# Performance work log

Hardware: AMD Instinct MI355X
Metric: run time of the kernel (lower is better)

The kernel has to match this reference:

```python
import jax, jax.numpy as jnp
import numpy as np

N_NODES = 50000
N_EDGES = 400000
HID = 64
NUM_REL = 230
NUM_TS = 365
SLOPE = 0.2  # LeakyReLU negative slope

def lrelu(v):
    return jnp.where(v >= 0, v, SLOPE * v)

def setup_inputs() -> dict:
    key = jax.random.key(0)
    ks = jax.random.split(key, 10)
    x = jax.random.normal(ks[0], (N_NODES, 2 * HID), dtype=jnp.float32)
    rel_table = jax.random.normal(ks[1], (NUM_REL, HID), dtype=jnp.float32) * 0.1
    time_table = jax.random.normal(ks[2], (NUM_TS, HID), dtype=jnp.float32) * 0.1
    W_rt = jax.random.normal(ks[3], (2 * HID, 2 * HID), dtype=jnp.float32) * (1.0 / np.sqrt(2 * HID))
    b_rt = jnp.zeros((2 * HID,), dtype=jnp.float32)
    W_fc = jax.random.normal(ks[4], (6 * HID, 2 * HID), dtype=jnp.float32) * (1.0 / np.sqrt(6 * HID))
    b_fc = jnp.zeros((2 * HID,), dtype=jnp.float32)
    src = jax.random.randint(ks[5], (N_EDGES,), 0, N_NODES)
    dst = jax.random.randint(ks[6], (N_EDGES,), 0, N_NODES)
    rel = jax.random.randint(ks[7], (N_EDGES,), 0, NUM_REL)
    ts = jax.random.randint(ks[8], (N_EDGES,), 0, NUM_TS)
    edges = jnp.stack([src, dst, rel, ts], axis=1).astype(jnp.int64) if jax.config.jax_enable_x64 else jnp.stack([src, dst, rel, ts], axis=1)
    return {
        "x": x, "rel_table": rel_table, "time_table": time_table,
        "W_rt": W_rt, "b_rt": b_rt, "W_fc": W_fc, "b_fc": b_fc,
        "edges": edges, "num_nodes": N_NODES,
    }

def reference(x, rel_table, time_table, W_rt, b_rt, W_fc, b_fc, edges, num_nodes):
    # MessagePassing.forward + LogicalGNN.aggregated_messages (scatter_mean)
    src, dst, rel, ts = edges[:, 0], edges[:, 1], edges[:, 2], edges[:, 3]
    rel_e = rel_table[rel]          # [E, H]
    time_e = time_table[ts]         # [E, H]
    rel_t = lrelu(jnp.concatenate([rel_e, time_e], axis=-1) @ W_rt + b_rt)  # [E, 2H]
    msg_in = jnp.concatenate([x[src], rel_t, x[dst]], axis=-1)              # [E, 6H]
    messages = lrelu(msg_in @ W_fc + b_fc)                                  # [E, 2H]
    # scatter_mean over dst
    sums = jax.ops.segment_sum(messages, dst, num_segments=num_nodes)       # [N, 2H]
    counts = jax.ops.segment_sum(jnp.ones((messages.shape[0],), messages.dtype), dst, num_segments=num_nodes)
    agg = sums / jnp.maximum(counts, 1.0)[:, None]
    return agg
```

## Files before the change

kernel.cpp:

```cpp
#include <hip/hip_runtime.h>
#include <cstdio>

#define HID 64
#define D 128
#define NUM_REL 230
#define NUM_TS 365
#define NCOMB (NUM_REL*NUM_TS)
#define SLOPE 0.2f
#define XPAD 136
#define MAXDEG 64

typedef __attribute__((ext_vector_type(8))) short short8;
typedef __attribute__((ext_vector_type(4))) float f32x4;

__device__ __forceinline__ float lrelu(float v){ return v >= 0.f ? v : SLOPE*v; }

__device__ __forceinline__ unsigned bf_rne(float f){
    unsigned u = __float_as_uint(f);
    return (u + 0x7fffu + ((u >> 16) & 1u)) >> 16;
}
__device__ __forceinline__ unsigned pk2(float a, float b){
    return bf_rne(a) | (bf_rne(b) << 16);
}
__device__ __forceinline__ float bf_lo(unsigned u){ return __uint_as_float(u << 16); }
__device__ __forceinline__ float bf_hi(unsigned u){ return __uint_as_float(u & 0xffff0000u); }

__global__ __launch_bounds__(256) void k_prep(
        const float* __restrict__ rel_table, const float* __restrict__ time_table,
        const float* __restrict__ W_rt, const float* __restrict__ W_fc,
        const int* __restrict__ edges, int n_edges,
        float* __restrict__ relP, float* __restrict__ timP,
        unsigned short* __restrict__ Wpk13, unsigned short* __restrict__ Wpk2,
        int* __restrict__ deg, int2* __restrict__ ebuf)
{
    int b = blockIdx.x;
    if (b < 298) {
        int row = b*2 + (threadIdx.x >> 7);
        int j   = threadIdx.x & 127;
        if (row >= NUM_REL + NUM_TS) return;
        const float* tbl; const float* Wb; float* out;
        if (row < NUM_REL) { tbl = rel_table + row*HID;            Wb = W_rt;          out = relP + row*D; }
        else               { tbl = time_table + (row-NUM_REL)*HID; Wb = W_rt + HID*D;  out = timP + (row-NUM_REL)*D; }
        float acc = 0.f;
        #pragma unroll
        for (int k = 0; k < HID; ++k) acc += tbl[k] * Wb[k*D + j];
        out[j] = acc;
    } else if (b < 322) {
        int id = (b - 298)*256 + threadIdx.x;
        if (id < 4096) {
            int mt = id >> 8;
            int s  = (id >> 6) & 3;
            int l  = id & 63;
            int m  = mt*16 + (l & 15);
            int kb = s*32 + (l >> 4)*8;
            unsigned short* dst = Wpk13 + ((size_t)(mt*4 + s)*64 + l)*8;
            #pragma unroll
            for (int j = 0; j < 8; ++j) {
                int k = kb + j;
                float v = (m < D) ? W_fc[(size_t)k*D + m]
                                  : W_fc[(size_t)(256 + k)*D + (m - D)];
                dst[j] = (unsigned short)bf_rne(v);
            }
        } else {
            int id2 = id - 4096;
            int mt = id2 >> 8;
            int s  = (id2 >> 6) & 3;
            int l  = id2 & 63;
            int m  = mt*16 + (l & 15);
            int kb = s*32 + (l >> 4)*8;
            unsigned short* dst = Wpk2 + ((size_t)(mt*4 + s)*64 + l)*8;
            #pragma unroll
            for (int j = 0; j < 8; ++j) {
                int k = kb + j;
                dst[j] = (unsigned short)bf_rne(W_fc[(size_t)(D + k)*D + m]);
            }
        }
    } else {
        int e = (b - 322)*256 + threadIdx.x;
        if (e < n_edges) {
            int4 ed = ((const int4*)edges)[e];
            int slot = atomicAdd(&deg[ed.y], 1);
            if (slot < MAXDEG)
                ebuf[(size_t)ed.y*MAXDEG + slot] = make_int2(ed.x, ed.z*NUM_TS + ed.w);
        }
    }
}

__device__ __forceinline__ void xw_body(
        int xb, const float* __restrict__ x,
        const unsigned short* __restrict__ Wpk13,
        unsigned short* __restrict__ xW13bf, int n_nodes,
        unsigned short* Xs )
{
    int t = threadIdx.x;
    int nodeBase = xb*64;
    {
        int row = t >> 2;
        int k0  = (t & 3)*32;
        int node = nodeBase + row;
        unsigned short* dst = Xs + row*XPAD + k0;
        if (node < n_nodes) {
            const float4* src = (const float4*)(x + (size_t)node*D + k0);
            #pragma unroll
            for (int g = 0; g < 8; ++g) {
                float4 v = src[g];
                *(uint2*)(dst + g*4) = make_uint2(pk2(v.x, v.y), pk2(v.z, v.w));
            }
        } else {
            #pragma unroll
            for (int g = 0; g < 8; ++g)
                *(uint2*)(dst + g*4) = make_uint2(0u, 0u);
        }
    }
    __syncthreads();

    int w = t >> 6, l = t & 63;
    int li = l & 15, q = l >> 4;

    f32x4 acc[4][4];
    #pragma unroll
    for (int mi = 0; mi < 4; ++mi)
        #pragma unroll
        for (int ni = 0; ni < 4; ++ni) acc[mi][ni] = (f32x4){0.f,0.f,0.f,0.f};

    #pragma unroll 1
    for (int s = 0; s < 4; ++s) {
        short8 af[4], bf[4];
        #pragma unroll
        for (int mi = 0; mi < 4; ++mi) {
            int mt = w*4 + mi;
            af[mi] = *(const short8*)(Wpk13 + ((size_t)(mt*4 + s)*64 + l)*8);
        }
        #pragma unroll
        for (int ni = 0; ni < 4; ++ni)
            bf[ni] = *(const short8*)(Xs + (ni*16 + li)*XPAD + s*32 + q*8);
        #pragma unroll
        for (int mi = 0; mi < 4; ++mi)
            #pragma unroll
            for (int ni = 0; ni < 4; ++ni)
                acc[mi][ni] = __builtin_amdgcn_mfma_f32_16x16x32_bf16(
                                  af[mi], bf[ni], acc[mi][ni], 0, 0, 0);
    }
    #pragma unroll
    for (int ni = 0; ni < 4; ++ni) {
        int node = nodeBase + ni*16 + li;
        if (node >= n_nodes) continue;
        #pragma unroll
        for (int mi = 0; mi < 4; ++mi) {
            int col = w*64 + mi*16 + q*4;
            *(uint2*)(xW13bf + (size_t)node*256 + col) =
                make_uint2(pk2(acc[mi][ni][0], acc[mi][ni][1]),
                           pk2(acc[mi][ni][2], acc[mi][ni][3]));
        }
    }
}

__device__ __forceinline__ void t2_body(
        int tb, const float* __restrict__ relP, const float* __restrict__ timP,
        const float* __restrict__ b_rt, const unsigned short* __restrict__ Wpk2,
        unsigned short* __restrict__ T2bf,
        unsigned short* Hs )
{
    int t = threadIdx.x;
    int cBase = tb*128;
    {
        int r  = t >> 1;
        int hk = (t & 1)*64;
        int combo = cBase + r;
        if (combo >= NCOMB) combo = NCOMB - 1;
        int rr = combo / NUM_TS;
        int tt = combo - rr*NUM_TS;
        const float4* rv4 = (const float4*)(relP + (size_t)rr*D + hk);
        const float4* tv4 = (const float4*)(timP + (size_t)tt*D + hk);
        const float4* bv4 = (const float4*)(b_rt + hk);
        unsigned short* dst = Hs + r*XPAD + hk;
        #pragma unroll
        for (int g = 0; g < 16; ++g) {
            float4 rv = rv4[g], tv = tv4[g], bv = bv4[g];
            float v0 = lrelu(rv.x+tv.x+bv.x), v1 = lrelu(rv.y+tv.y+bv.y);
            float v2 = lrelu(rv.z+tv.z+bv.z), v3 = lrelu(rv.w+tv.w+bv.w);
            *(uint2*)(dst + g*4) = make_uint2(pk2(v0,v1), pk2(v2,v3));
        }
    }
    __syncthreads();

    int w = t >> 6, l = t & 63;
    int li = l & 15, q = l >> 4;
    int mb = (w & 1)*4;
    int nb = (w >> 1)*64;

    f32x4 acc[4][4];
    #pragma unroll
    for (int mi = 0; mi < 4; ++mi)
        #pragma unroll
        for (int ni = 0; ni < 4; ++ni) acc[mi][ni] = (f32x4){0.f,0.f,0.f,0.f};

    #pragma unroll 1
    for (int s = 0; s < 4; ++s) {
        short8 af[4], bf[4];
        #pragma unroll
        for (int mi = 0; mi < 4; ++mi)
            af[mi] = *(const short8*)(Wpk2 + ((size_t)((mb+mi)*4 + s)*64 + l)*8);
        #pragma unroll
        for (int ni = 0; ni < 4; ++ni)
            bf[ni] = *(const short8*)(Hs + (nb + ni*16 + li)*XPAD + s*32 + q*8);
        #pragma unroll
        for (int mi = 0; mi < 4; ++mi)
            #pragma unroll
            for (int ni = 0; ni < 4; ++ni)
                acc[mi][ni] = __builtin_amdgcn_mfma_f32_16x16x32_bf16(
                                  af[mi], bf[ni], acc[mi][ni], 0, 0, 0);
    }
    #pragma unroll
    for (int ni = 0; ni < 4; ++ni) {
        int combo = cBase + nb + ni*16 + li;
        if (combo >= NCOMB) continue;
        #pragma unroll
        for (int mi = 0; mi < 4; ++mi) {
            int col = (mb + mi)*16 + q*4;
            *(uint2*)(T2bf + (size_t)combo*D + col) =
                make_uint2(pk2(acc[mi][ni][0], acc[mi][ni][1]),
                           pk2(acc[mi][ni][2], acc[mi][ni][3]));
        }
    }
}

__global__ __launch_bounds__(256, 3) void k_mm(
        const float* __restrict__ x, const unsigned short* __restrict__ Wpk13,
        unsigned short* __restrict__ xW13bf, int n_nodes,
        const float* __restrict__ relP, const float* __restrict__ timP,
        const float* __restrict__ b_rt, const unsigned short* __restrict__ Wpk2,
        unsigned short* __restrict__ T2bf, int nxw)
{
    __shared__ __align__(16) unsigned short Hs[128*XPAD];
    int b = blockIdx.x;
    if (b < nxw) {
        xw_body(b, x, Wpk13, xW13bf, n_nodes, Hs);
    } else {
        t2_body(b - nxw, relP, timP, b_rt, Wpk2, T2bf, Hs);
    }
}

__global__ __launch_bounds__(256) void k_agg(
        const int* __restrict__ deg, const int2* __restrict__ ebuf,
        const unsigned short* __restrict__ xW13bf,
        const unsigned short* __restrict__ T2bf,
        const float* __restrict__ b_fc,
        float* __restrict__ out, int n_nodes)
{
    int node = blockIdx.x*4 + (threadIdx.x >> 6);
    int lane = threadIdx.x & 63;
    if (node >= n_nodes) return;
    int dg  = deg[node];
    int cnt = dg < MAXDEG ? dg : MAXDEG;
    const int2* eb = ebuf + (size_t)node*MAXDEG;

    float2 bb = *(const float2*)&b_fc[2*lane];
    unsigned xw3 = *(const unsigned*)&xW13bf[(size_t)node*256 + 128 + 2*lane];
    float base0 = bf_lo(xw3) + bb.x;
    float base1 = bf_hi(xw3) + bb.y;

    float s0 = 0.f, s1 = 0.f;
    float r0 = 0.f, r1 = 0.f;

    for (int e = 0; e < cnt; e += 16) {
        int m = cnt - e;
        int2 ed[16]; unsigned sv[16], tv[16];
        #pragma unroll
        for (int j = 0; j < 16; ++j)
            if (j < m) ed[j] = eb[e + j];
        #pragma unroll
        for (int j = 0; j < 16; ++j)
            if (j < m) {
                sv[j] = *(const unsigned*)&xW13bf[(size_t)ed[j].x*256 + 2*lane];
                tv[j] = *(const unsigned*)&T2bf  [(size_t)ed[j].y*D   + 2*lane];
            }
        #pragma unroll
        for (int j = 0; j < 16; ++j)
            if (j < m) {
                if (j & 1) {
                    r0 += lrelu(bf_lo(sv[j]) + bf_lo(tv[j]) + base0);
                    r1 += lrelu(bf_hi(sv[j]) + bf_hi(tv[j]) + base1);
                } else {
                    s0 += lrelu(bf_lo(sv[j]) + bf_lo(tv[j]) + base0);
                    s1 += lrelu(bf_hi(sv[j]) + bf_hi(tv[j]) + base1);
                }
            }
    }
    float inv = 1.f / fmaxf((float)dg, 1.f);
    *(float2*)&out[(size_t)node*D + 2*lane] =
        make_float2((s0 + r0)*inv, (s1 + r1)*inv);
}

extern "C" void kernel_launch(void* const* d_in, const int* in_sizes, int n_in,
                              void* d_out, int out_size, void* d_ws, size_t ws_size,
                              hipStream_t stream)
{
    const float* x          = (const float*)d_in[0];
    const float* rel_table  = (const float*)d_in[1];
    const float* time_table = (const float*)d_in[2];
    const float* W_rt       = (const float*)d_in[3];
    const float* b_rt       = (const float*)d_in[4];
    const float* W_fc       = (const float*)d_in[5];
    const float* b_fc       = (const float*)d_in[6];
    const int*   edges      = (const int*)d_in[7];

    int n_nodes = in_sizes[0] / D;
    int n_edges = in_sizes[7] / 4;
    int nblkE   = (n_edges + 255) / 256;
    int nxw     = (n_nodes + 63) / 64;
    int nt2     = (NCOMB + 127) / 128;

    char* ws = (char*)d_ws;
    size_t off = 0;
    auto alloc = [&](size_t bytes) -> void* {
        void* p = ws + off; off += (bytes + 255) & ~(size_t)255; return p;
    };
    unsigned short* xW13bf = (unsigned short*)alloc((size_t)n_nodes * 256 * 2);
    unsigned short* T2bf   = (unsigned short*)alloc((size_t)NCOMB * D * 2);
    unsigned short* Wpk13  = (unsigned short*)alloc((size_t)16*4*64*8 * 2);
    unsigned short* Wpk2   = (unsigned short*)alloc((size_t)8*4*64*8 * 2);
    float* relP   = (float*)alloc((size_t)NUM_REL * D * sizeof(float));
    float* timP   = (float*)alloc((size_t)NUM_TS * D * sizeof(float));
    int*   deg    = (int*)alloc((size_t)n_nodes * sizeof(int));
    int2*  ebuf   = (int2*)alloc((size_t)n_nodes * MAXDEG * sizeof(int2));
    if (off > ws_size)
        fprintf(stderr, "kernel_launch: workspace too small: need %zu, have %zu\n", off, ws_size);

    hipMemsetAsync(deg, 0, (size_t)n_nodes * sizeof(int), stream);

    k_prep<<<322 + nblkE, 256, 0, stream>>>(rel_table, time_table, W_rt, W_fc,
                                            edges, n_edges,
                                            relP, timP, Wpk13, Wpk2, deg, ebuf);
    k_mm  <<<nxw + nt2, 256, 0, stream>>>(x, Wpk13, xW13bf, n_nodes,
                                          relP, timP, b_rt, Wpk2, T2bf, nxw);
    k_agg <<<(n_nodes + 3)/4, 256, 0, stream>>>(deg, ebuf, xW13bf, T2bf,
                                                b_fc, (float*)d_out, n_nodes);
}
```

Baseline: 202.1 us.

## Process four nodes per wavefront with 16-byte vector gathers in aggregation

The aggregation kernel now maps 16 lanes to each destination node, so one wavefront handles four nodes. Each lane gathers 16-byte chunks (8 bf16 values) of the source projection and the relation-time table instead of 4-byte words. Edge loops run to the wavefront's max degree, with clamped indices and masking, so all lanes take the same path. This cuts the number of memory instructions and should improve gather efficiency, but lanes on low-degree nodes do wasted work when degrees differ within a wavefront.

```diff
diff --git a/kernel.cpp b/kernel.cpp
--- a/kernel.cpp
+++ b/kernel.cpp
@@ -248,48 +248,89 @@
         const float* __restrict__ b_fc,
         float* __restrict__ out, int n_nodes)
 {
-    int node = blockIdx.x*4 + (threadIdx.x >> 6);
-    int lane = threadIdx.x & 63;
-    if (node >= n_nodes) return;
-    int dg  = deg[node];
-    int cnt = dg < MAXDEG ? dg : MAXDEG;
-    const int2* eb = ebuf + (size_t)node*MAXDEG;
-
-    float2 bb = *(const float2*)&b_fc[2*lane];
-    unsigned xw3 = *(const unsigned*)&xW13bf[(size_t)node*256 + 128 + 2*lane];
-    float base0 = bf_lo(xw3) + bb.x;
-    float base1 = bf_hi(xw3) + bb.y;
-
-    float s0 = 0.f, s1 = 0.f;
-    float r0 = 0.f, r1 = 0.f;
-
-    for (int e = 0; e < cnt; e += 16) {
-        int m = cnt - e;
-        int2 ed[16]; unsigned sv[16], tv[16];
-        #pragma unroll
-        for (int j = 0; j < 16; ++j)
-            if (j < m) ed[j] = eb[e + j];
-        #pragma unroll
-        for (int j = 0; j < 16; ++j)
-            if (j < m) {
-                sv[j] = *(const unsigned*)&xW13bf[(size_t)ed[j].x*256 + 2*lane];
-                tv[j] = *(const unsigned*)&T2bf  [(size_t)ed[j].y*D   + 2*lane];
-            }
-        #pragma unroll
-        for (int j = 0; j < 16; ++j)
-            if (j < m) {
-                if (j & 1) {
-                    r0 += lrelu(bf_lo(sv[j]) + bf_lo(tv[j]) + base0);
-                    r1 += lrelu(bf_hi(sv[j]) + bf_hi(tv[j]) + base1);
-                } else {
-                    s0 += lrelu(bf_lo(sv[j]) + bf_lo(tv[j]) + base0);
-                    s1 += lrelu(bf_hi(sv[j]) + bf_hi(tv[j]) + base1);
-                }
-            }
-    }
+    int t    = threadIdx.x;
+    int lane = t & 63;
+    int g    = lane >> 4;
+    int sub  = lane & 15;
+    int node = blockIdx.x*16 + (t >> 6)*4 + g;
+    bool valid = node < n_nodes;
+    int nodeC  = valid ? node : n_nodes - 1;
+
+    int dg  = deg[nodeC];
+    int cnt = valid ? (dg < MAXDEG ? dg : MAXDEG) : 0;
+    int cm1 = cnt > 0 ? cnt - 1 : 0;
+    const int2* eb = ebuf + (size_t)nodeC * MAXDEG;
+
+    int cmax = cnt;
+    cmax = max(cmax, __shfl_xor(cmax, 16));
+    cmax = max(cmax, __shfl_xor(cmax, 32));
+
+    float base[8];
+    {
+        uint4  w3  = *(const uint4*)&xW13bf[(size_t)nodeC*256 + 128 + sub*8];
+        float4 blo = *(const float4*)&b_fc[sub*8];
+        float4 bhi = *(const float4*)&b_fc[sub*8 + 4];
+        base[0] = bf_lo(w3.x) + blo.x; base[1] = bf_hi(w3.x) + blo.y;
+        base[2] = bf_lo(w3.y) + blo.z; base[3] = bf_hi(w3.y) + blo.w;
+        base[4] = bf_lo(w3.z) + bhi.x; base[5] = bf_hi(w3.z) + bhi.y;
+        base[6] = bf_lo(w3.w) + bhi.z; base[7] = bf_hi(w3.w) + bhi.w;
+    }
+
+    float acc[8];
+    #pragma unroll
+    for (int k = 0; k < 8; ++k) acc[k] = 0.f;
+
+    const unsigned sMax = (unsigned)(n_nodes - 1);
+    const unsigned cMax = (unsigned)(NCOMB - 1);
+
+    for (int e = 0; e < cmax; e += 4) {
+        int2 e0 = eb[min(e + 0, cm1)];
+        int2 e1 = eb[min(e + 1, cm1)];
+        int2 e2 = eb[min(e + 2, cm1)];
+        int2 e3 = eb[min(e + 3, cm1)];
+        unsigned s0 = min((unsigned)e0.x, sMax), c0 = min((unsigned)e0.y, cMax);
+        unsigned s1 = min((unsigned)e1.x, sMax), c1 = min((unsigned)e1.y, cMax);
+        unsigned s2 = min((unsigned)e2.x, sMax), c2 = min((unsigned)e2.y, cMax);
+        unsigned s3 = min((unsigned)e3.x, sMax), c3 = min((unsigned)e3.y, cMax);
+        uint4 S0 = *(const uint4*)&xW13bf[(size_t)s0*256 + sub*8];
+        uint4 T0 = *(const uint4*)&T2bf  [(size_t)c0*D   + sub*8];
+        uint4 S1 = *(const uint4*)&xW13bf[(size_t)s1*256 + sub*8];
+        uint4 T1 = *(const uint4*)&T2bf  [(size_t)c1*D   + sub*8];
+        uint4 S2 = *(const uint4*)&xW13bf[(size_t)s2*256 + sub*8];
+        uint4 T2 = *(const uint4*)&T2bf  [(size_t)c2*D   + sub*8];
+        uint4 S3 = *(const uint4*)&xW13bf[(size_t)s3*256 + sub*8];
+        uint4 T3 = *(const uint4*)&T2bf  [(size_t)c3*D   + sub*8];
+        bool m0 = (e + 0) < cnt, m1 = (e + 1) < cnt;
+        bool m2 = (e + 2) < cnt, m3 = (e + 3) < cnt;
+        #pragma unroll
+        for (int w = 0; w < 4; ++w) {
+            unsigned Sw0 = (&S0.x)[w], Tw0 = (&T0.x)[w];
+            unsigned Sw1 = (&S1.x)[w], Tw1 = (&T1.x)[w];
+            unsigned Sw2 = (&S2.x)[w], Tw2 = (&T2.x)[w];
+            unsigned Sw3 = (&S3.x)[w], Tw3 = (&T3.x)[w];
+            float v0l = lrelu(bf_lo(Sw0) + bf_lo(Tw0) + base[2*w]);
+            float v0h = lrelu(bf_hi(Sw0) + bf_hi(Tw0) + base[2*w+1]);
+            float v1l = lrelu(bf_lo(Sw1) + bf_lo(Tw1) + base[2*w]);
+            float v1h = lrelu(bf_hi(Sw1) + bf_hi(Tw1) + base[2*w+1]);
+            float v2l = lrelu(bf_lo(Sw2) + bf_lo(Tw2) + base[2*w]);
+            float v2h = lrelu(bf_hi(Sw2) + bf_hi(Tw2) + base[2*w+1]);
+            float v3l = lrelu(bf_lo(Sw3) + bf_lo(Tw3) + base[2*w]);
+            float v3h = lrelu(bf_hi(Sw3) + bf_hi(Tw3) + base[2*w+1]);
+            float a01l = (m0 ? v0l : 0.f) + (m1 ? v1l : 0.f);
+            float a23l = (m2 ? v2l : 0.f) + (m3 ? v3l : 0.f);
+            float a01h = (m0 ? v0h : 0.f) + (m1 ? v1h : 0.f);
+            float a23h = (m2 ? v2h : 0.f) + (m3 ? v3h : 0.f);
+            acc[2*w]   += a01l + a23l;
+            acc[2*w+1] += a01h + a23h;
+        }
+    }
+
+    if (!valid) return;
     float inv = 1.f / fmaxf((float)dg, 1.f);
-    *(float2*)&out[(size_t)node*D + 2*lane] =
-        make_float2((s0 + r0)*inv, (s1 + r1)*inv);
+    float4 o0 = make_float4(acc[0]*inv, acc[1]*inv, acc[2]*inv, acc[3]*inv);
+    float4 o1 = make_float4(acc[4]*inv, acc[5]*inv, acc[6]*inv, acc[7]*inv);
+    *(float4*)&out[(size_t)node*D + sub*8]     = o0;
+    *(float4*)&out[(size_t)node*D + sub*8 + 4] = o1;
 }
 
 extern "C" void kernel_launch(void* const* d_in, const int* in_sizes, int n_in,
@@ -334,6 +375,6 @@
                                             relP, timP, Wpk13, Wpk2, deg, ebuf);
     k_mm  <<<nxw + nt2, 256, 0, stream>>>(x, Wpk13, xW13bf, n_nodes,
                                           relP, timP, b_rt, Wpk2, T2bf, nxw);
-    k_agg <<<(n_nodes + 3)/4, 256, 0, stream>>>(deg, ebuf, xW13bf, T2bf,
-                                                b_fc, (float*)d_out, n_nodes);
-}
+    k_agg <<<(n_nodes + 15)/16, 256, 0, stream>>>(deg, ebuf, xW13bf, T2bf,
+                                                  b_fc, (float*)d_out, n_nodes);
+}
```

Result: faster. 179.7 us (-11.1%).
